# Kernel optimization log

Hardware: AMD Instinct MI355X
Metric: run time of the kernel (lower is better)

The kernel has to match this reference:

```python
import jax, jax.numpy as jnp
import numpy as np

N_NODES = 100000
N_EDGES = 1600000
D_FEAT = 128
HIDDEN = 256


def setup_inputs() -> dict:
    key = jax.random.key(0)
    k1, k2, k3, k4, k5, k6, k7 = jax.random.split(key, 7)
    h = jax.random.normal(k1, (N_NODES, D_FEAT), dtype=jnp.float32)
    src = jax.random.randint(k2, (N_EDGES,), 0, N_NODES, dtype=jnp.int64)
    dst = jax.random.randint(k3, (N_EDGES,), 0, N_NODES, dtype=jnp.int64)
    # Linear weights, torch layout: W [out, in], b [out]
    lim1 = 1.0 / np.sqrt(2 * D_FEAT)
    W1_w = jax.random.uniform(k4, (HIDDEN, 2 * D_FEAT), minval=-lim1, maxval=lim1, dtype=jnp.float32)
    W1_b = jax.random.uniform(k5, (HIDDEN,), minval=-lim1, maxval=lim1, dtype=jnp.float32)
    lim2 = 1.0 / np.sqrt(HIDDEN)
    W2_w = jax.random.uniform(k6, (1, HIDDEN), minval=-lim2, maxval=lim2, dtype=jnp.float32)
    W2_b = jax.random.uniform(k7, (1,), minval=-lim2, maxval=lim2, dtype=jnp.float32)
    return {"h": h, "src": src, "dst": dst, "W1_w": W1_w, "W1_b": W1_b, "W2_w": W2_w, "W2_b": W2_b}


def reference(h, src, dst, W1_w, W1_b, W2_w, W2_b):
    # gather per-edge src/dst node features and concat: [E, 2D]
    x = jnp.concatenate([h[src], h[dst]], axis=1)
    # Linear -> ReLU -> Linear, squeeze last dim -> [E]
    hid = jax.nn.relu(x @ W1_w.T + W1_b)          # [E, H]
    score = (hid @ W2_w.T + W2_b)[:, 0]           # [E]
    return score
```

## Files before the change

kernel.cpp:

```cpp
#include <hip/hip_runtime.h>


#define NNODES 100000
#define E_TOTAL 1600000
#define D 128
#define K2 256
#define H 256
#define NB2 49
#define EDGE_GRID 3125
#define SORT_GRID 256
#define EPB (E_TOTAL / SORT_GRID)
#define GT_ROWS 128

typedef short bf16x8 __attribute__((ext_vector_type(8)));
typedef float f32x4 __attribute__((ext_vector_type(4)));
typedef const __attribute__((address_space(1))) unsigned short* gas_t;
typedef __attribute__((address_space(3))) unsigned short* las_t;

__device__ __forceinline__ unsigned short f2bf(float f) {
    unsigned u = __float_as_uint(f);
    u += 0x7fff + ((u >> 16) & 1);
    return (unsigned short)(u >> 16);
}
__device__ __forceinline__ float bf2f(unsigned short s) {
    return __uint_as_float((unsigned)s << 16);
}

__device__ __forceinline__ int xcd_chunk(int orig, int nwg) {
    const int q = nwg >> 3, r = nwg & 7;
    const int x = orig & 7, s = orig >> 3;
    return (x < r ? x * (q + 1) : r * (q + 1) + (x - r) * q) + s;
}

__global__ void cvt_kernel(const float* __restrict__ h, const float* __restrict__ w1,
                           unsigned short* __restrict__ hbf, unsigned short* __restrict__ w1bf,
                           int n4h, int n4w,
                           const int* __restrict__ srcE, int* __restrict__ cnt, int nCvt) {
    __shared__ int lh[NB2];
    const int tid = threadIdx.x;
    if ((int)blockIdx.x >= nCvt) {
        const int k = blockIdx.x - nCvt;
        const int base = k * EPB;
        if (tid < NB2) lh[tid] = 0;
        __syncthreads();
        for (int i = tid; i < EPB; i += 256)
            atomicAdd(&lh[srcE[base + i] >> 11], 1);
        __syncthreads();
        if (tid < NB2) cnt[k * NB2 + tid] = lh[tid];
        return;
    }
    int i = blockIdx.x * blockDim.x + tid;
    if (i >= n4h + n4w) return;
    const float* s; unsigned short* d; int j;
    if (i < n4h) { s = h; d = hbf; j = i; }
    else { s = w1; d = w1bf; j = i - n4h; }
    float4 v = ((const float4*)s)[j];
    ushort4 o;
    o.x = f2bf(v.x); o.y = f2bf(v.y); o.z = f2bf(v.z); o.w = f2bf(v.w);
    ((ushort4*)d)[j] = o;
}

__global__ __launch_bounds__(256, 3) void u_gemm4(
    const unsigned short* __restrict__ hbf,
    const unsigned short* __restrict__ w1bf,
    const float* __restrict__ b1,
    unsigned short* __restrict__ Us,
    unsigned short* __restrict__ Ud)
{
    __shared__ __align__(16) unsigned short A[GT_ROWS * 128];

    const int tid = threadIdx.x;
    const int wave = tid >> 6;
    const int lane = tid & 63;
    const int l15 = lane & 15;
    const int quad = lane >> 4;

    const int tile = blockIdx.x >> 2;
    const int half = (blockIdx.x >> 1) & 1;
    const int nh = blockIdx.x & 1;
    const int r0 = tile * GT_ROWS;
    int rows = NNODES - r0; if (rows > GT_ROWS) rows = GT_ROWS;
    const int koff = half * 128;
    unsigned short* U = half ? Ud : Us;

#pragma unroll
    for (int it = 0; it < 8; ++it) {
        const int s = it * 256 + tid;
        const int r = s >> 4;
        const int p = s & 15;
        const int c = p ^ (r & 15);
        if (r < rows)
            __builtin_amdgcn_global_load_lds(
                (gas_t)(hbf + (size_t)(r0 + r) * D + c * 8),
                (las_t)(A + it * 2048 + wave * 512), 16, 0, 0);
    }

    bf16x8 B[4][2];
    float bias[2];
#pragma unroll
    for (int nt = 0; nt < 2; ++nt) {
        const int n = nh * 128 + wave * 32 + nt * 16 + l15;
        bias[nt] = half ? 0.f : b1[n];
#pragma unroll
        for (int kit = 0; kit < 4; ++kit)
            B[kit][nt] = *(const bf16x8*)(w1bf + (size_t)n * K2 + koff + kit * 32 + quad * 8);
    }

    __syncthreads();

    f32x4 acc[8][2];
    const f32x4 zero = {0.f, 0.f, 0.f, 0.f};
#pragma unroll
    for (int ms = 0; ms < 8; ++ms)
#pragma unroll
        for (int nt = 0; nt < 2; ++nt)
            acc[ms][nt] = zero;

#pragma unroll
    for (int kit = 0; kit < 4; ++kit) {
        const int p = (kit * 4 + quad) ^ l15;
#pragma unroll
        for (int ms = 0; ms < 8; ++ms) {
            const int row = ms * 16 + l15;
            const bf16x8 a = *(const bf16x8*)&A[row * 128 + p * 8];
#pragma unroll
            for (int nt = 0; nt < 2; ++nt)
                acc[ms][nt] = __builtin_amdgcn_mfma_f32_16x16x32_bf16(
                    a, B[kit][nt], acc[ms][nt], 0, 0, 0);
        }
    }

    const int coff = nh * 128 + wave * 32 + l15 * 2;
#pragma unroll
    for (int ms = 0; ms < 8; ++ms) {
#pragma unroll
        for (int r = 0; r < 4; ++r) {
            const int m = ms * 16 + quad * 4 + r;
            if (m < rows) {
                const unsigned lo = f2bf(acc[ms][0][r] + bias[0]);
                const unsigned hi = f2bf(acc[ms][1][r] + bias[1]);
                *(unsigned*)(U + (size_t)(r0 + m) * H + coff) = lo | (hi << 16);
            }
        }
    }
}

__global__ __launch_bounds__(256) void scatter49(
    const int* __restrict__ srcE, const int* __restrict__ dstE,
    const int* __restrict__ cnt,
    unsigned long long* __restrict__ pk, int* __restrict__ rank)
{
    __shared__ int pref[NB2];
    __shared__ int lcur[NB2];
    const int tid = threadIdx.x;
    const int k = blockIdx.x;
    const int base = k * EPB;

    if (tid < NB2) {
        int lb = 0, tot = 0;
        for (int kk = 0; kk < SORT_GRID; ++kk) {
            const int c = cnt[kk * NB2 + tid];
            if (kk < k) lb += c;
            tot += c;
        }
        lcur[tid] = lb;
        pref[tid] = tot;
    }
    __syncthreads();
    if (tid == 0) {
        int s = 0;
        for (int b = 0; b < NB2; ++b) { const int t = pref[b]; pref[b] = s; s += t; }
    }
    __syncthreads();
    if (tid < NB2) lcur[tid] += pref[tid];
    __syncthreads();

    for (int i = tid; i < EPB; i += 256) {
        const int e = base + i;
        const int s = srcE[e];
        const int d = dstE[e];
        const int b = s >> 11;
        const int p = atomicAdd(&lcur[b], 1);
        pk[(size_t)p] = (unsigned long long)s | ((unsigned long long)d << 17);
        rank[e] = p;
    }
}

__global__ __launch_bounds__(256) void edge_score_pk(
    const unsigned short* __restrict__ Us,
    const unsigned short* __restrict__ Ud,
    const unsigned long long* __restrict__ pk,
    const float* __restrict__ w2,
    const float* __restrict__ b2p,
    float* __restrict__ ssort)
{
    const int b = xcd_chunk(blockIdx.x, gridDim.x);
    const int tid = threadIdx.x;
    const int l = tid & 15;
    const int grp = b * 16 + (tid >> 4);

    float w2v[16];
#pragma unroll
    for (int j = 0; j < 16; ++j) {
        const int cp = l * 16 + j;
        const int n = (cp & ~31) + ((cp & 1) << 4) + ((cp & 31) >> 1);
        w2v[j] = w2[n];
    }
    const float b2 = *b2p;

    const int g0 = grp * 8;
    for (int g = g0; g < g0 + 8; ++g) {
        const int e0 = g * 4;
        const uint4 pa = *(const uint4*)(pk + e0);
        const uint4 pb = *(const uint4*)(pk + e0 + 2);
        const unsigned lo[4] = {pa.x, pa.z, pb.x, pb.z};
        const unsigned hi[4] = {pa.y, pa.w, pb.y, pb.w};
        int sv[4], dv[4];
#pragma unroll
        for (int k = 0; k < 4; ++k) {
            sv[k] = lo[k] & 0x1FFFF;
            dv[k] = ((lo[k] >> 17) | (hi[k] << 15)) & 0x1FFFF;
        }

        bf16x8 u[4][2], v[4][2];
#pragma unroll
        for (int k = 0; k < 4; ++k) {
            const bf16x8* us = (const bf16x8*)(Us + (size_t)sv[k] * H + l * 16);
            const bf16x8* ud = (const bf16x8*)(Ud + (size_t)dv[k] * H + l * 16);
            u[k][0] = us[0]; u[k][1] = us[1];
            v[k][0] = ud[0]; v[k][1] = ud[1];
        }

        float4 res;
        float* resp = (float*)&res;
#pragma unroll
        for (int k = 0; k < 4; ++k) {
            float acc = 0.f;
#pragma unroll
            for (int j = 0; j < 8; ++j) {
                float hv = bf2f((unsigned short)u[k][0][j]) + bf2f((unsigned short)v[k][0][j]);
                acc = fmaf(fmaxf(hv, 0.f), w2v[j], acc);
            }
#pragma unroll
            for (int j = 0; j < 8; ++j) {
                float hv = bf2f((unsigned short)u[k][1][j]) + bf2f((unsigned short)v[k][1][j]);
                acc = fmaf(fmaxf(hv, 0.f), w2v[j + 8], acc);
            }
            acc += __shfl_xor(acc, 1, 16);
            acc += __shfl_xor(acc, 2, 16);
            acc += __shfl_xor(acc, 4, 16);
            acc += __shfl_xor(acc, 8, 16);
            resp[k] = acc + b2;
        }
        if (l == 0) *(float4*)(ssort + e0) = res;
    }
}

__global__ __launch_bounds__(256) void unscatter(
    const float* __restrict__ ssort, const int* __restrict__ rank,
    float* __restrict__ out)
{
    const int g = blockIdx.x * 256 + threadIdx.x;
    if (g >= E_TOTAL / 4) return;
    const int e0 = g * 4;
    const int4 r4 = *(const int4*)(rank + e0);
    float4 o;
    o.x = ssort[r4.x];
    o.y = ssort[r4.y];
    o.z = ssort[r4.z];
    o.w = ssort[r4.w];
    *(float4*)(out + e0) = o;
}

__global__ __launch_bounds__(256) void edge_score(
    const unsigned short* __restrict__ Us,
    const unsigned short* __restrict__ Ud,
    const int* __restrict__ srcE,
    const int* __restrict__ dstE,
    const float* __restrict__ w2,
    const float* __restrict__ b2p,
    float* __restrict__ out)
{
    const int gt = blockIdx.x * 256 + threadIdx.x;
    const int l = gt & 15;
    const int q = gt >> 4;
    const int Q = (gridDim.x * 256) >> 4;
    const int NGRP = E_TOTAL / 4;

    float w2v[16];
#pragma unroll
    for (int j = 0; j < 16; ++j) {
        const int cp = l * 16 + j;
        const int n = (cp & ~31) + ((cp & 1) << 4) + ((cp & 31) >> 1);
        w2v[j] = w2[n];
    }
    const float b2 = *b2p;

    for (int g = q; g < NGRP; g += Q) {
        const int e0 = g * 4;
        const int4 s4 = *(const int4*)(srcE + e0);
        const int4 d4 = *(const int4*)(dstE + e0);
        const int sv[4] = {s4.x, s4.y, s4.z, s4.w};
        const int dv[4] = {d4.x, d4.y, d4.z, d4.w};

        bf16x8 u[4][2], v[4][2];
#pragma unroll
        for (int k = 0; k < 4; ++k) {
            const bf16x8* us = (const bf16x8*)(Us + (size_t)sv[k] * H + l * 16);
            const bf16x8* ud = (const bf16x8*)(Ud + (size_t)dv[k] * H + l * 16);
            u[k][0] = us[0]; u[k][1] = us[1];
            v[k][0] = ud[0]; v[k][1] = ud[1];
        }

        float4 res;
        float* resp = (float*)&res;
#pragma unroll
        for (int k = 0; k < 4; ++k) {
            float acc = 0.f;
#pragma unroll
            for (int j = 0; j < 8; ++j) {
                float hv = bf2f((unsigned short)u[k][0][j]) + bf2f((unsigned short)v[k][0][j]);
                acc = fmaf(fmaxf(hv, 0.f), w2v[j], acc);
            }
#pragma unroll
            for (int j = 0; j < 8; ++j) {
                float hv = bf2f((unsigned short)u[k][1][j]) + bf2f((unsigned short)v[k][1][j]);
                acc = fmaf(fmaxf(hv, 0.f), w2v[j + 8], acc);
            }
            acc += __shfl_xor(acc, 1, 16);
            acc += __shfl_xor(acc, 2, 16);
            acc += __shfl_xor(acc, 4, 16);
            acc += __shfl_xor(acc, 8, 16);
            resp[k] = acc + b2;
        }
        if (l == 0) *(float4*)(out + e0) = res;
    }
}


#define TILE_M 32
#define NTILES (E_TOTAL / TILE_M)
#define GRID 2500

#if defined(__has_attribute)
#if __has_attribute(amdgpu_waves_per_eu)
#define LB __launch_bounds__(256) __attribute__((amdgpu_waves_per_eu(2, 2)))
#else
#define LB __launch_bounds__(256, 2)
#endif
#else
#define LB __launch_bounds__(256, 2)
#endif

__global__ LB void edge_mlp(
    const unsigned short* __restrict__ hbf,
    const int* __restrict__ srcE,
    const int* __restrict__ dstE,
    const unsigned short* __restrict__ w1bf,
    const float* __restrict__ b1,
    const float* __restrict__ w2,
    const float* __restrict__ b2p,
    float* __restrict__ out)
{
    __shared__ __align__(16) unsigned short X[2][TILE_M * K2];
    __shared__ float red[2][TILE_M][5];

    const int tid = threadIdx.x;
    const int wave = tid >> 6;
    const int lane = tid & 63;
    const int lane15 = lane & 15;
    const int quad = lane >> 4;

    bf16x8 B[8][4];
#pragma unroll
    for (int kit = 0; kit < 8; ++kit)
#pragma unroll
        for (int nt = 0; nt < 4; ++nt) {
            int n = wave * 64 + nt * 16 + lane15;
            int k = kit * 32 + quad * 8;
            B[kit][nt] = *(const bf16x8*)(w1bf + n * K2 + k);
        }

    float b1v[4], w2v[4];
#pragma unroll
    for (int nt = 0; nt < 4; ++nt) {
        int n = wave * 64 + nt * 16 + lane15;
        b1v[nt] = b1[n];
        w2v[nt] = w2[n];
    }
    const float b2 = *b2p;

    const int r_off = tid >> 5;
    const int c = (tid & 31) ^ (r_off & 7);
    const int half = c >> 4;
    const int fc = c & 15;
    const int* idx_base = half ? dstE : srcE;
    const int gshort = fc * 8;

    const int t0 = blockIdx.x;
    int inode[4];

#pragma unroll
    for (int it = 0; it < 4; ++it)
        inode[it] = idx_base[t0 * TILE_M + it * 8 + r_off];
#pragma unroll
    for (int it = 0; it < 4; ++it)
        __builtin_amdgcn_global_load_lds(
            (gas_t)(hbf + inode[it] * D + gshort),
            (las_t)(&X[0][0] + it * 2048 + wave * 512), 16, 0, 0);
    {
        const int t1 = t0 + GRID;
#pragma unroll
        for (int it = 0; it < 4; ++it)
            inode[it] = idx_base[t1 * TILE_M + it * 8 + r_off];
    }

    int buf = 0;
    int prev_eb = -1;

    for (int tile = t0; tile < NTILES; tile += GRID) {
        __syncthreads();

        const int nt1 = tile + GRID;
        if (nt1 < NTILES) {
            unsigned short* Xn = &X[buf ^ 1][0];
#pragma unroll
            for (int it = 0; it < 4; ++it)
                __builtin_amdgcn_global_load_lds(
                    (gas_t)(hbf + inode[it] * D + gshort),
                    (las_t)(Xn + it * 2048 + wave * 512), 16, 0, 0);
        }
        const int nt2 = tile + 2 * GRID;
        if (nt2 < NTILES) {
            const int eb2 = nt2 * TILE_M;
#pragma unroll
            for (int it = 0; it < 4; ++it)
                inode[it] = idx_base[eb2 + it * 8 + r_off];
        }
        if (prev_eb >= 0 && tid < TILE_M) {
            float s = b2;
#pragma unroll
            for (int w = 0; w < 4; ++w) s += red[buf ^ 1][tid][w];
            out[prev_eb + tid] = s;
        }

        const unsigned short* Xc = &X[buf][0];
        f32x4 acc[2][4];
        const f32x4 zero = {0.f, 0.f, 0.f, 0.f};
#pragma unroll
        for (int ms = 0; ms < 2; ++ms)
#pragma unroll
            for (int nt = 0; nt < 4; ++nt)
                acc[ms][nt] = zero;

#pragma unroll
        for (int kit = 0; kit < 8; ++kit) {
            const int p8 = (((kit * 4 + quad) ^ (lane15 & 7))) * 8;
            bf16x8 a[2];
#pragma unroll
            for (int ms = 0; ms < 2; ++ms)
                a[ms] = *(const bf16x8*)&Xc[(ms * 16 + lane15) * K2 + p8];
#pragma unroll
            for (int ms = 0; ms < 2; ++ms)
#pragma unroll
                for (int nt = 0; nt < 4; ++nt)
                    acc[ms][nt] = __builtin_amdgcn_mfma_f32_16x16x32_bf16(
                        a[ms], B[kit][nt], acc[ms][nt], 0, 0, 0);
        }

#pragma unroll
        for (int ms = 0; ms < 2; ++ms)
#pragma unroll
            for (int r = 0; r < 4; ++r) {
                float p = 0.f;
#pragma unroll
                for (int nt = 0; nt < 4; ++nt) {
                    float hv = acc[ms][nt][r] + b1v[nt];
                    p = fmaf(fmaxf(hv, 0.f), w2v[nt], p);
                }
                p += __shfl_xor(p, 1, 16);
                p += __shfl_xor(p, 2, 16);
                p += __shfl_xor(p, 4, 16);
                p += __shfl_xor(p, 8, 16);
                if (lane15 == 0) red[buf][ms * 16 + quad * 4 + r][wave] = p;
            }
        prev_eb = tile * TILE_M;
        buf ^= 1;
    }

    __syncthreads();
    if (prev_eb >= 0 && tid < TILE_M) {
        float s = b2;
#pragma unroll
        for (int w = 0; w < 4; ++w) s += red[buf ^ 1][tid][w];
        out[prev_eb + tid] = s;
    }
}


extern "C" void kernel_launch(void* const* d_in, const int* in_sizes, int n_in,
                              void* d_out, int out_size, void* d_ws, size_t ws_size,
                              hipStream_t stream) {
    const float* h    = (const float*)d_in[0];
    const int*   srcE = (const int*)d_in[1];
    const int*   dstE = (const int*)d_in[2];
    const float* W1   = (const float*)d_in[3];
    const float* b1   = (const float*)d_in[4];
    const float* w2   = (const float*)d_in[5];
    const float* b2   = (const float*)d_in[6];
    float* out = (float*)d_out;

    char* ws = (char*)d_ws;
    const size_t offUs   = 0;
    const size_t offUd   = 51200000;
    const size_t offHbf  = 102400000;
    const size_t offW1bf = 128000000;
    const size_t need    = offW1bf + 131072;
    const size_t offCnt  = need;
    const size_t offPK   = offCnt + 65536;
    const size_t need2   = offPK + 12800000;

    if (ws_size >= need) {
        unsigned short* Us   = (unsigned short*)(ws + offUs);
        unsigned short* Ud   = (unsigned short*)(ws + offUd);
        unsigned short* hbf  = (unsigned short*)(ws + offHbf);
        unsigned short* w1bf = (unsigned short*)(ws + offW1bf);
        const bool sorted = (ws_size >= need2);
        int* cnt = (int*)(ws + offCnt);
        unsigned long long* pk = (unsigned long long*)(ws + offPK);
        int*   rank  = (int*)(ws + offHbf);
        float* ssort = (float*)(ws + offHbf + 6400000);

        int n4h = NNODES * D / 4, n4w = H * K2 / 4;
        const int nCvt = (n4h + n4w + 255) / 256;
        const int cvtGrid = nCvt + (sorted ? SORT_GRID : 0);
        cvt_kernel<<<cvtGrid, 256, 0, stream>>>(
            h, W1, hbf, w1bf, n4h, n4w, srcE, cnt, nCvt);
        u_gemm4<<<4 * ((NNODES + GT_ROWS - 1) / GT_ROWS), 256, 0, stream>>>(
            hbf, w1bf, b1, Us, Ud);
        if (sorted) {
            scatter49<<<SORT_GRID, 256, 0, stream>>>(srcE, dstE, cnt, pk, rank);
            edge_score_pk<<<EDGE_GRID, 256, 0, stream>>>(Us, Ud, pk, w2, b2, ssort);
            unscatter<<<(E_TOTAL / 4 + 255) / 256, 256, 0, stream>>>(ssort, rank, out);
        } else {
            edge_score<<<4096, 256, 0, stream>>>(Us, Ud, srcE, dstE, w2, b2, out);
        }
    } else {
        unsigned short* hbf  = (unsigned short*)d_ws;
        unsigned short* w1bf = hbf + (size_t)NNODES * D;
        int n4h = NNODES * D / 4, n4w = H * K2 / 4;
        cvt_kernel<<<(n4h + n4w + 255) / 256, 256, 0, stream>>>(
            h, W1, hbf, w1bf, n4h, n4w, nullptr, nullptr, (n4h + n4w + 255) / 256);
        edge_mlp<<<GRID, 256, 0, stream>>>(hbf, srcE, dstE, w1bf, b1, w2, b2, out);
    }
}
```

Measured before the change: 335.7 us.

## Fuse fp32-to-bf16 conversion into node GEMM and drop separate convert kernel

The standalone conversion kernel that wrote bf16 copies of h and W1 is removed. The node-level GEMM now loads fp32 h directly into LDS, converts to bf16 in registers before each MFMA, and converts W1 fragments on load. The src-histogram blocks are appended to the GEMM launch. The tile shrinks from 128 to 64 rows so the fp32 tile fits in the same LDS budget. This saves one kernel launch and the write and re-read of the bf16 h copy, at the cost of more LDS traffic, per-use conversion work and twice as many W1 fragment loads across blocks.

```diff
diff --git a/kernel.cpp b/kernel.cpp
--- a/kernel.cpp
+++ b/kernel.cpp
@@ -10,12 +10,13 @@
 #define EDGE_GRID 3125
 #define SORT_GRID 256
 #define EPB (E_TOTAL / SORT_GRID)
-#define GT_ROWS 128
 
 typedef short bf16x8 __attribute__((ext_vector_type(8)));
 typedef float f32x4 __attribute__((ext_vector_type(4)));
 typedef const __attribute__((address_space(1))) unsigned short* gas_t;
 typedef __attribute__((address_space(3))) unsigned short* las_t;
+typedef const __attribute__((address_space(1))) float* gasf_t;
+typedef __attribute__((address_space(3))) float* lasf_t;
 
 __device__ __forceinline__ unsigned short f2bf(float f) {
     unsigned u = __float_as_uint(f);
@@ -25,6 +26,14 @@
 __device__ __forceinline__ float bf2f(unsigned short s) {
     return __uint_as_float((unsigned)s << 16);
 }
+__device__ __forceinline__ bf16x8 cvt8(const float4 f0, const float4 f1) {
+    bf16x8 b;
+    b[0] = (short)f2bf(f0.x); b[1] = (short)f2bf(f0.y);
+    b[2] = (short)f2bf(f0.z); b[3] = (short)f2bf(f0.w);
+    b[4] = (short)f2bf(f1.x); b[5] = (short)f2bf(f1.y);
+    b[6] = (short)f2bf(f1.z); b[7] = (short)f2bf(f1.w);
+    return b;
+}
 
 __device__ __forceinline__ int xcd_chunk(int orig, int nwg) {
     const int q = nwg >> 3, r = nwg & 7;
@@ -32,14 +41,23 @@
     return (x < r ? x * (q + 1) : r * (q + 1) + (x - r) * q) + s;
 }
 
-__global__ void cvt_kernel(const float* __restrict__ h, const float* __restrict__ w1,
-                           unsigned short* __restrict__ hbf, unsigned short* __restrict__ w1bf,
-                           int n4h, int n4w,
-                           const int* __restrict__ srcE, int* __restrict__ cnt, int nCvt) {
+__global__ __launch_bounds__(256, 3) void u_gemm5(
+    const float* __restrict__ h,
+    const float* __restrict__ w1,
+    const float* __restrict__ b1,
+    unsigned short* __restrict__ Us,
+    unsigned short* __restrict__ Ud,
+    const int* __restrict__ srcE,
+    int* __restrict__ cnt,
+    int nBody)
+{
+    __shared__ __align__(16) float Af[64 * 128];
     __shared__ int lh[NB2];
+
     const int tid = threadIdx.x;
-    if ((int)blockIdx.x >= nCvt) {
-        const int k = blockIdx.x - nCvt;
+
+    if ((int)blockIdx.x >= nBody) {
+        const int k = blockIdx.x - nBody;
         const int base = k * EPB;
         if (tid < NB2) lh[tid] = 0;
         __syncthreads();
@@ -49,27 +67,7 @@
         if (tid < NB2) cnt[k * NB2 + tid] = lh[tid];
         return;
     }
-    int i = blockIdx.x * blockDim.x + tid;
-    if (i >= n4h + n4w) return;
-    const float* s; unsigned short* d; int j;
-    if (i < n4h) { s = h; d = hbf; j = i; }
-    else { s = w1; d = w1bf; j = i - n4h; }
-    float4 v = ((const float4*)s)[j];
-    ushort4 o;
-    o.x = f2bf(v.x); o.y = f2bf(v.y); o.z = f2bf(v.z); o.w = f2bf(v.w);
-    ((ushort4*)d)[j] = o;
-}
-
-__global__ __launch_bounds__(256, 3) void u_gemm4(
-    const unsigned short* __restrict__ hbf,
-    const unsigned short* __restrict__ w1bf,
-    const float* __restrict__ b1,
-    unsigned short* __restrict__ Us,
-    unsigned short* __restrict__ Ud)
-{
-    __shared__ __align__(16) unsigned short A[GT_ROWS * 128];
-
-    const int tid = threadIdx.x;
+
     const int wave = tid >> 6;
     const int lane = tid & 63;
     const int l15 = lane & 15;
@@ -78,21 +76,22 @@
     const int tile = blockIdx.x >> 2;
     const int half = (blockIdx.x >> 1) & 1;
     const int nh = blockIdx.x & 1;
-    const int r0 = tile * GT_ROWS;
-    int rows = NNODES - r0; if (rows > GT_ROWS) rows = GT_ROWS;
+    const int r0 = tile * 64;
+    int rows = NNODES - r0; if (rows > 64) rows = 64;
     const int koff = half * 128;
     unsigned short* U = half ? Ud : Us;
 
 #pragma unroll
     for (int it = 0; it < 8; ++it) {
         const int s = it * 256 + tid;
-        const int r = s >> 4;
-        const int p = s & 15;
-        const int c = p ^ (r & 15);
+        const int r = s >> 5;
+        const int pg = (s >> 1) & 15;
+        const int t = s & 1;
+        const int cg = pg ^ (r & 15);
         if (r < rows)
             __builtin_amdgcn_global_load_lds(
-                (gas_t)(hbf + (size_t)(r0 + r) * D + c * 8),
-                (las_t)(A + it * 2048 + wave * 512), 16, 0, 0);
+                (gasf_t)(h + (size_t)(r0 + r) * D + cg * 8 + t * 4),
+                (lasf_t)(Af + it * 1024 + wave * 256), 16, 0, 0);
     }
 
     bf16x8 B[4][2];
@@ -102,27 +101,33 @@
         const int n = nh * 128 + wave * 32 + nt * 16 + l15;
         bias[nt] = half ? 0.f : b1[n];
 #pragma unroll
-        for (int kit = 0; kit < 4; ++kit)
-            B[kit][nt] = *(const bf16x8*)(w1bf + (size_t)n * K2 + koff + kit * 32 + quad * 8);
+        for (int kit = 0; kit < 4; ++kit) {
+            const float* src = w1 + (size_t)n * K2 + koff + kit * 32 + quad * 8;
+            const float4 f0 = *(const float4*)src;
+            const float4 f1 = *(const float4*)(src + 4);
+            B[kit][nt] = cvt8(f0, f1);
+        }
     }
 
     __syncthreads();
 
-    f32x4 acc[8][2];
+    f32x4 acc[4][2];
     const f32x4 zero = {0.f, 0.f, 0.f, 0.f};
 #pragma unroll
-    for (int ms = 0; ms < 8; ++ms)
+    for (int ms = 0; ms < 4; ++ms)
 #pragma unroll
         for (int nt = 0; nt < 2; ++nt)
             acc[ms][nt] = zero;
 
 #pragma unroll
     for (int kit = 0; kit < 4; ++kit) {
-        const int p = (kit * 4 + quad) ^ l15;
-#pragma unroll
-        for (int ms = 0; ms < 8; ++ms) {
+        const int g = (kit * 4 + quad) ^ l15;
+#pragma unroll
+        for (int ms = 0; ms < 4; ++ms) {
             const int row = ms * 16 + l15;
-            const bf16x8 a = *(const bf16x8*)&A[row * 128 + p * 8];
+            const float4 f0 = *(const float4*)&Af[row * 128 + g * 8];
+            const float4 f1 = *(const float4*)&Af[row * 128 + g * 8 + 4];
+            const bf16x8 a = cvt8(f0, f1);
 #pragma unroll
             for (int nt = 0; nt < 2; ++nt)
                 acc[ms][nt] = __builtin_amdgcn_mfma_f32_16x16x32_bf16(
@@ -132,7 +137,7 @@
 
     const int coff = nh * 128 + wave * 32 + l15 * 2;
 #pragma unroll
-    for (int ms = 0; ms < 8; ++ms) {
+    for (int ms = 0; ms < 4; ++ms) {
 #pragma unroll
         for (int r = 0; r < 4; ++r) {
             const int m = ms * 16 + quad * 4 + r;
@@ -338,6 +343,20 @@
 }
 
 
+__global__ void cvt_kernel(const float* __restrict__ h, const float* __restrict__ w1,
+                           unsigned short* __restrict__ hbf, unsigned short* __restrict__ w1bf,
+                           int n4h, int n4w) {
+    int i = blockIdx.x * blockDim.x + threadIdx.x;
+    if (i >= n4h + n4w) return;
+    const float* s; unsigned short* d; int j;
+    if (i < n4h) { s = h; d = hbf; j = i; }
+    else { s = w1; d = w1bf; j = i - n4h; }
+    float4 v = ((const float4*)s)[j];
+    ushort4 o;
+    o.x = f2bf(v.x); o.y = f2bf(v.y); o.z = f2bf(v.z); o.w = f2bf(v.w);
+    ((ushort4*)d)[j] = o;
+}
+
 #define TILE_M 32
 #define NTILES (E_TOTAL / TILE_M)
 #define GRID 2500
@@ -511,46 +530,42 @@
     float* out = (float*)d_out;
 
     char* ws = (char*)d_ws;
-    const size_t offUs   = 0;
-    const size_t offUd   = 51200000;
-    const size_t offHbf  = 102400000;
-    const size_t offW1bf = 128000000;
-    const size_t need    = offW1bf + 131072;
-    const size_t offCnt  = need;
-    const size_t offPK   = offCnt + 65536;
-    const size_t need2   = offPK + 12800000;
-
-    if (ws_size >= need) {
-        unsigned short* Us   = (unsigned short*)(ws + offUs);
-        unsigned short* Ud   = (unsigned short*)(ws + offUd);
-        unsigned short* hbf  = (unsigned short*)(ws + offHbf);
-        unsigned short* w1bf = (unsigned short*)(ws + offW1bf);
-        const bool sorted = (ws_size >= need2);
-        int* cnt = (int*)(ws + offCnt);
+    const size_t offUs    = 0;
+    const size_t offUd    = 51200000;
+    const size_t offRank  = 102400000;
+    const size_t offSsort = 108800000;
+    const size_t offCnt   = 115200000;
+    const size_t offPK    = 115265536;
+    const size_t needSort = offPK + 12800000;
+    const size_t needMid  = 102400000;
+
+    const int nBody = 4 * ((NNODES + 63) / 64);
+
+    if (ws_size >= needSort) {
+        unsigned short* Us = (unsigned short*)(ws + offUs);
+        unsigned short* Ud = (unsigned short*)(ws + offUd);
+        int*   rank  = (int*)(ws + offRank);
+        float* ssort = (float*)(ws + offSsort);
+        int*   cnt   = (int*)(ws + offCnt);
         unsigned long long* pk = (unsigned long long*)(ws + offPK);
-        int*   rank  = (int*)(ws + offHbf);
-        float* ssort = (float*)(ws + offHbf + 6400000);
-
-        int n4h = NNODES * D / 4, n4w = H * K2 / 4;
-        const int nCvt = (n4h + n4w + 255) / 256;
-        const int cvtGrid = nCvt + (sorted ? SORT_GRID : 0);
-        cvt_kernel<<<cvtGrid, 256, 0, stream>>>(
-            h, W1, hbf, w1bf, n4h, n4w, srcE, cnt, nCvt);
-        u_gemm4<<<4 * ((NNODES + GT_ROWS - 1) / GT_ROWS), 256, 0, stream>>>(
-            hbf, w1bf, b1, Us, Ud);
-        if (sorted) {
-            scatter49<<<SORT_GRID, 256, 0, stream>>>(srcE, dstE, cnt, pk, rank);
-            edge_score_pk<<<EDGE_GRID, 256, 0, stream>>>(Us, Ud, pk, w2, b2, ssort);
-            unscatter<<<(E_TOTAL / 4 + 255) / 256, 256, 0, stream>>>(ssort, rank, out);
-        } else {
-            edge_score<<<4096, 256, 0, stream>>>(Us, Ud, srcE, dstE, w2, b2, out);
-        }
+
+        u_gemm5<<<nBody + SORT_GRID, 256, 0, stream>>>(
+            h, W1, b1, Us, Ud, srcE, cnt, nBody);
+        scatter49<<<SORT_GRID, 256, 0, stream>>>(srcE, dstE, cnt, pk, rank);
+        edge_score_pk<<<EDGE_GRID, 256, 0, stream>>>(Us, Ud, pk, w2, b2, ssort);
+        unscatter<<<(E_TOTAL / 4 + 255) / 256, 256, 0, stream>>>(ssort, rank, out);
+    } else if (ws_size >= needMid) {
+        unsigned short* Us = (unsigned short*)(ws + offUs);
+        unsigned short* Ud = (unsigned short*)(ws + offUd);
+        u_gemm5<<<nBody, 256, 0, stream>>>(
+            h, W1, b1, Us, Ud, srcE, nullptr, nBody);
+        edge_score<<<4096, 256, 0, stream>>>(Us, Ud, srcE, dstE, w2, b2, out);
     } else {
         unsigned short* hbf  = (unsigned short*)d_ws;
         unsigned short* w1bf = hbf + (size_t)NNODES * D;
         int n4h = NNODES * D / 4, n4w = H * K2 / 4;
         cvt_kernel<<<(n4h + n4w + 255) / 256, 256, 0, stream>>>(
-            h, W1, hbf, w1bf, n4h, n4w, nullptr, nullptr, (n4h + n4w + 255) / 256);
+            h, W1, hbf, w1bf, n4h, n4w);
         edge_mlp<<<GRID, 256, 0, stream>>>(hbf, srcE, dstE, w1bf, b1, w2, b2, out);
     }
 }
```

Result: slower. 359.1 us (+7.0%).
